# Kernel tuning notes

Hardware: AMD Instinct MI355X
Metric: run time of the kernel (lower is better)

## Reference

```python
import jax, jax.numpy as jnp
import numpy as np

LOCAL_RADIUS = 127          # block_len = 128
TOKENS_PER_BLOCK = 16       # global_seq_len = L // 16
NEG = -1e9


def _concat_3_blocks(x):
    # x: [B, nb, bl, H, d] -> [B, nb, 3*bl, H, d] (prev, cur, next block; zero-padded ends)
    p = jnp.pad(x, [(0, 0), (1, 1), (0, 0), (0, 0), (0, 0)])
    return jnp.concatenate([p[:, :-2], p[:, 1:-1], p[:, 2:]], axis=2)


def _softmax_with_extra_logit(x, axis=-1):
    m = jnp.maximum(jax.lax.stop_gradient(x.max(axis, keepdims=True)), 0)
    unnorm = jnp.exp(x - m)
    denom = unnorm.sum(axis, keepdims=True) + jnp.exp(-m)
    return unnorm / denom


def setup_inputs() -> dict:
    key = jax.random.key(0)
    ks = jax.random.split(key, 5)
    B, L, D, H, dh = 2, 4096, 1024, 16, 64
    return {
        "x": jax.random.normal(ks[0], (B, L, D), jnp.float32),
        "Wq": jax.random.normal(ks[1], (D, H, dh), jnp.float32) * 0.02,
        "Wk": jax.random.normal(ks[2], (D, H, dh), jnp.float32) * 0.02,
        "Wv": jax.random.normal(ks[3], (D, H, dh), jnp.float32) * 0.02,
        "Wo": jax.random.normal(ks[4], (H, dh, D), jnp.float32) * 0.02,
    }


def reference(x, Wq, Wk, Wv, Wo):
    B, L, D = x.shape
    H, dh = Wq.shape[1], Wq.shape[2]
    bl = LOCAL_RADIUS + 1                      # block_len = 128
    nb = L // bl                               # num_blocks
    G = L // TOKENS_PER_BLOCK                  # global (side) seq len

    q = jnp.einsum("bld,dhk->blhk", x, Wq) / jnp.sqrt(jnp.asarray(dh, x.dtype))
    k = jnp.einsum("bld,dhk->blhk", x, Wk)
    v = jnp.einsum("bld,dhk->blhk", x, Wv)

    # transient-global aggregates: sum token embeddings within each block of TOKENS_PER_BLOCK
    block_ids = jnp.arange(L) // TOKENS_PER_BLOCK          # [L]
    one_hot = jax.nn.one_hot(block_ids, G, dtype=x.dtype)  # [L, G]
    g = jnp.einsum("bld,lg->bgd", x, one_hot)              # [B, G, D]
    side_k = jnp.einsum("bgd,dhk->bghk", g, Wk)
    side_v = jnp.einsum("bgd,dhk->bghk", g, Wv)

    # split into blocks and build 3-block sliding window keys/values
    qb = q.reshape(B, nb, bl, H, dh)
    kb = _concat_3_blocks(k.reshape(B, nb, bl, H, dh))     # [B, nb, 3bl, H, dh]
    vb = _concat_3_blocks(v.reshape(B, nb, bl, H, dh))

    k_cat = jnp.concatenate(
        [kb, jnp.broadcast_to(side_k[:, None], (B, nb, G, H, dh))], axis=2)
    v_cat = jnp.concatenate(
        [vb, jnp.broadcast_to(side_v[:, None], (B, nb, G, H, dh))], axis=2)

    # logits: [B, nb, H, bl, 3bl+G]
    logits = jnp.einsum("bnqhd,bnkhd->bnhqk", qb, k_cat)

    # local mask: enforce |rel| <= local_radius and in-bounds key positions
    q_idx = jnp.arange(bl)[:, None]                        # [bl, 1]
    k_idx = jnp.arange(3 * bl)[None, :]                    # [1, 3bl]
    rel = k_idx - bl - q_idx                               # relative position
    b_idx = jnp.arange(nb)[:, None, None]                  # [nb, 1, 1]
    k_pos = (b_idx - 1) * bl + k_idx                       # absolute key position
    valid = (jnp.abs(rel) <= LOCAL_RADIUS) & (k_pos >= 0) & (k_pos < L)
    local_bias = jnp.where(valid, 0.0, NEG).astype(logits.dtype)  # [nb, bl, 3bl]
    side_bias = jnp.zeros((nb, bl, G), logits.dtype)
    bias = jnp.concatenate([local_bias, side_bias], axis=-1)      # [nb, bl, 3bl+G]
    logits = logits + bias[None, :, None]

    probs = _softmax_with_extra_logit(logits, axis=-1)
    y = jnp.einsum("bnhqk,bnkhd->bnqhd", probs, v_cat)
    y = y.reshape(B, L, H, dh)
    return jnp.einsum("blhk,hkd->bld", y, Wo)
```

## Files before the change

### kernel.cpp

```cpp
#include <hip/hip_runtime.h>
#include <stdint.h>

#define SC_LOG2E 0.18033688011112042f

typedef __attribute__((ext_vector_type(8))) short short8;
typedef __attribute__((ext_vector_type(4))) float f32x4;

__device__ __forceinline__ unsigned short f2bf(float f) {
  unsigned int u = __float_as_uint(f);
  u += 0x7fffu + ((u >> 16) & 1u);
  return (unsigned short)(u >> 16);
}

__device__ __forceinline__ void gload_lds16(const void* g, void* l) {
  __builtin_amdgcn_global_load_lds((const __attribute__((address_space(1))) void*)g,
                                   (__attribute__((address_space(3))) void*)l,
                                   16, 0, 0);
}

__device__ __forceinline__ f32x4 mfma16(short8 a, short8 b, f32x4 c) {
  return __builtin_amdgcn_mfma_f32_16x16x32_bf16(a, b, c, 0, 0, 0);
}


__global__ __launch_bounds__(256) void prep_x_k(const float* __restrict__ x,
                                                unsigned short* __restrict__ xb,
                                                unsigned short* __restrict__ gb) {
  int gr = blockIdx.x;
  int c4 = threadIdx.x;
  const float4* p = (const float4*)(x + (size_t)gr * 16384) + c4;
  float4 s = {0.f, 0.f, 0.f, 0.f};
#pragma unroll
  for (int t = 0; t < 16; ++t) {
    float4 v = p[(size_t)t * 256];
    ushort4 o;
    o.x = f2bf(v.x); o.y = f2bf(v.y); o.z = f2bf(v.z); o.w = f2bf(v.w);
    ((ushort4*)xb)[(size_t)(gr * 16 + t) * 256 + c4] = o;
    s.x += v.x; s.y += v.y; s.z += v.z; s.w += v.w;
  }
  ushort4 og;
  og.x = f2bf(s.x); og.y = f2bf(s.y); og.z = f2bf(s.z); og.w = f2bf(s.w);
  ((ushort4*)gb)[(size_t)gr * 256 + c4] = og;
}

__global__ __launch_bounds__(256) void transpose_w4_k(
    const float* __restrict__ wq, const float* __restrict__ wk,
    const float* __restrict__ wv, const float* __restrict__ wo,
    unsigned short* __restrict__ wqkv_t, unsigned short* __restrict__ wo_t) {
  __shared__ float tile[64 * 65];
  int z = blockIdx.z;
  const float* src = (z == 0) ? wq : (z == 1) ? wk : (z == 2) ? wv : wo;
  unsigned short* dst = (z == 3) ? wo_t : (wqkv_t + (size_t)z * 1048576);
  float scale = (z == 0) ? SC_LOG2E : 1.0f;
  int tc = blockIdx.x * 64, tr = blockIdx.y * 64;
  int cx = threadIdx.x & 63, ry = threadIdx.x >> 6;
#pragma unroll
  for (int i = 0; i < 16; ++i) {
    int r = ry + i * 4;
    tile[r * 65 + cx] = src[(size_t)(tr + r) * 1024 + tc + cx];
  }
  __syncthreads();
#pragma unroll
  for (int i = 0; i < 16; ++i) {
    int r = ry + i * 4;
    dst[(size_t)(tc + r) * 1024 + tr + cx] = f2bf(tile[cx * 65 + r] * scale);
  }
}

__global__ __launch_bounds__(256) void transpose_bf16_k(
    const unsigned short* __restrict__ src, int sstride, size_t szstride,
    unsigned short* __restrict__ dst, int dstride, size_t dzstride) {
  __shared__ unsigned short tile[64 * 65];
  src += blockIdx.z * szstride;
  dst += blockIdx.z * dzstride;
  int tc = blockIdx.x * 64, tr = blockIdx.y * 64;
  int cx = threadIdx.x & 63, ry = threadIdx.x >> 6;
#pragma unroll
  for (int i = 0; i < 16; ++i) {
    int r = ry + i * 4;
    tile[r * 65 + cx] = src[(size_t)(tr + r) * sstride + tc + cx];
  }
  __syncthreads();
#pragma unroll
  for (int i = 0; i < 16; ++i) {
    int r = ry + i * 4;
    dst[(size_t)(tc + r) * dstride + tr + cx] = tile[cx * 65 + r];
  }
}

template <bool F32OUT>
__global__ __launch_bounds__(256) void gemm_bt_k(
    const unsigned short* __restrict__ A, const unsigned short* __restrict__ Bt,
    void* __restrict__ Cv, int M, int N, int K, int nbn) {
  __shared__ unsigned short Alds[128 * 64];
  __shared__ unsigned short Blds[128 * 64];
  int bid = blockIdx.x;
  int bm = bid / nbn, bn = bid % nbn;
  int lane = threadIdx.x & 63, wid = threadIdx.x >> 6;
  int wr = wid >> 1, wc = wid & 1;
  int l15 = lane & 15, lg = lane >> 4;

  f32x4 zero4 = {0.f, 0.f, 0.f, 0.f};
  f32x4 acc[4][4];
#pragma unroll
  for (int i = 0; i < 4; ++i)
#pragma unroll
    for (int j = 0; j < 4; ++j) acc[i][j] = zero4;

  int srow[4], scol[4];
#pragma unroll
  for (int i = 0; i < 4; ++i) {
    int seg = wid * 4 + i;
    int r = seg * 8 + (lane >> 3);
    srow[i] = r;
    scol[i] = ((lane & 7) ^ (r & 7)) * 8;
  }
  size_t arow0 = (size_t)bm * 128, brow0 = (size_t)bn * 128;

  int ksteps = K >> 6;
  for (int ks = 0; ks < ksteps; ++ks) {
    int k0 = ks << 6;
#pragma unroll
    for (int i = 0; i < 4; ++i) {
      gload_lds16(A + (arow0 + srow[i]) * K + k0 + scol[i],
                  (char*)Alds + (wid * 4 + i) * 1024);
      gload_lds16(Bt + (brow0 + srow[i]) * K + k0 + scol[i],
                  (char*)Blds + (wid * 4 + i) * 1024);
    }
    __syncthreads();
#pragma unroll
    for (int kk = 0; kk < 2; ++kk) {
      short8 af[4], bfr[4];
#pragma unroll
      for (int mi = 0; mi < 4; ++mi) {
        int r = wr * 64 + mi * 16 + l15;
        af[mi] = *(const short8*)((const char*)Alds + r * 128 +
                                  ((kk * 64 + lg * 16) ^ ((r & 7) << 4)));
      }
#pragma unroll
      for (int ni = 0; ni < 4; ++ni) {
        int r = wc * 64 + ni * 16 + l15;
        bfr[ni] = *(const short8*)((const char*)Blds + r * 128 +
                                   ((kk * 64 + lg * 16) ^ ((r & 7) << 4)));
      }
#pragma unroll
      for (int mi = 0; mi < 4; ++mi)
#pragma unroll
        for (int ni = 0; ni < 4; ++ni)
          acc[mi][ni] = mfma16(af[mi], bfr[ni], acc[mi][ni]);
    }
    __syncthreads();
  }
  int rq = lg << 2;
#pragma unroll
  for (int mi = 0; mi < 4; ++mi) {
    size_t row = arow0 + wr * 64 + mi * 16 + rq;
#pragma unroll
    for (int ni = 0; ni < 4; ++ni) {
      size_t col = brow0 + wc * 64 + ni * 16 + l15;
#pragma unroll
      for (int r = 0; r < 4; ++r) {
        if (F32OUT)
          ((float*)Cv)[(row + r) * N + col] = acc[mi][ni][r];
        else
          ((unsigned short*)Cv)[(row + r) * N + col] = f2bf(acc[mi][ni][r]);
      }
    }
  }
}

__global__ __launch_bounds__(256) void attn_k(
    const unsigned short* __restrict__ qkv,
    const unsigned short* __restrict__ side_kv,
    const unsigned short* __restrict__ v_t,
    const unsigned short* __restrict__ side_v_t,
    unsigned short* __restrict__ y) {
  const int L = 4096, G = 256;
  __shared__ unsigned short K0[4096], V0[4096];
  __shared__ unsigned short K1[4096], V1[4096];
  __shared__ unsigned short Pl[4][2048];

  int bid = blockIdx.x;
  int n = bid & 31, h = (bid >> 5) & 15, b = bid >> 9;
  int lane = threadIdx.x & 63, wid = threadIdx.x >> 6;
  int l15 = lane & 15, lg = lane >> 4, rq = lg << 2;

  short8 qf[2][2];
  {
    size_t rowb = (size_t)b * L + n * 128 + wid * 32;
#pragma unroll
    for (int qt = 0; qt < 2; ++qt)
#pragma unroll
      for (int kk = 0; kk < 2; ++kk)
        qf[qt][kk] = *(const short8*)(qkv + (rowb + qt * 16 + l15) * 3072 +
                                      h * 64 + kk * 32 + lg * 8);
  }

  f32x4 zero4 = {0.f, 0.f, 0.f, 0.f};
  f32x4 accO[2][4], accSum[2];
#pragma unroll
  for (int qt = 0; qt < 2; ++qt) {
    accSum[qt] = zero4;
#pragma unroll
    for (int dt = 0; dt < 4; ++dt) accO[qt][dt] = zero4;
  }

  short8 onesf;
  {
    short o = (l15 == 0) ? (short)0x3F80 : (short)0;
    onesf = (short8){o, o, o, o, o, o, o, o};
  }

  int clo = (n == 0) ? 2 : 0, chi = (n == 31) ? 4 : 6;
  int nloc = chi - clo, goff = 6 - nloc;
  int m = nloc + 4;
  unsigned short* pw = Pl[wid];

  auto stage = [&](int c, unsigned short* Kl, unsigned short* Vl) {
    bool isg = c >= 6;
#pragma unroll
    for (int i = 0; i < 2; ++i) {
      int seg = wid * 2 + i;
      int r = seg * 8 + (lane >> 3);
      int sl = ((lane & 7) ^ (r & 7)) * 8;
      const unsigned short *ksrc, *vsrc;
      if (!isg) {
        int p0 = (n - 1) * 128 + c * 64;
        ksrc = qkv + (size_t)(b * L + p0 + r) * 3072 + 1024 + h * 64 + sl;
        vsrc = v_t + ((size_t)b * 1024 + h * 64 + r) * L + p0 + sl;
      } else {
        int g0 = (c - 6) * 64;
        ksrc = side_kv + (size_t)(b * G + g0 + r) * 2048 + h * 64 + sl;
        vsrc = side_v_t + ((size_t)b * 1024 + h * 64 + r) * G + g0 + sl;
      }
      gload_lds16(ksrc, (char*)Kl + seg * 1024);
      gload_lds16(vsrc, (char*)Vl + seg * 1024);
    }
  };

  auto compute = [&](int c, const unsigned short* Kl, const unsigned short* Vl) {
    bool isg = c >= 6;
    int d0 = c * 64 - 128 - wid * 32;
    if (!isg) {
      if (d0 >= 159 || d0 <= -191) return;
    }
    bool partial = !isg && !(d0 >= -96 && d0 <= 64);

    f32x4 sacc[2][4];
#pragma unroll
    for (int qt = 0; qt < 2; ++qt)
#pragma unroll
      for (int kt = 0; kt < 4; ++kt) sacc[qt][kt] = zero4;
#pragma unroll
    for (int kk = 0; kk < 2; ++kk) {
      short8 kf[4];
#pragma unroll
      for (int kt = 0; kt < 4; ++kt) {
        int r = kt * 16 + l15;
        kf[kt] = *(const short8*)((const char*)Kl + r * 128 +
                                  ((kk * 64 + lg * 16) ^ ((r & 7) << 4)));
      }
#pragma unroll
      for (int qt = 0; qt < 2; ++qt)
#pragma unroll
        for (int kt = 0; kt < 4; ++kt)
          sacc[qt][kt] = mfma16(qf[qt][kk], kf[kt], sacc[qt][kt]);
    }
    if (partial) {
      int relc = d0 + l15 - rq;
#pragma unroll
      for (int qt = 0; qt < 2; ++qt)
#pragma unroll
        for (int kt = 0; kt < 4; ++kt)
#pragma unroll
          for (int r = 0; r < 4; ++r) {
            int rel = relc + kt * 16 - qt * 16 - r;
            sacc[qt][kt][r] =
                ((unsigned)(rel + 127) <= 254u) ? sacc[qt][kt][r] : -1e30f;
          }
    }
#pragma unroll
    for (int qt = 0; qt < 2; ++qt)
#pragma unroll
      for (int kt = 0; kt < 4; ++kt)
#pragma unroll
        for (int r = 0; r < 4; ++r) {
          float p = __builtin_amdgcn_exp2f(sacc[qt][kt][r]);
          int row = qt * 16 + rq + r;
          int cb = (kt * 16 + l15) * 2;
          *(unsigned short*)((char*)pw + row * 128 +
                             (cb ^ ((row & 7) << 4))) = f2bf(p);
        }
#pragma unroll
    for (int ks = 0; ks < 2; ++ks) {
      short8 pa[2], vb[4];
#pragma unroll
      for (int qt = 0; qt < 2; ++qt) {
        int row = qt * 16 + l15;
        pa[qt] = *(const short8*)((const char*)pw + row * 128 +
                                  ((ks * 64 + lg * 16) ^ ((row & 7) << 4)));
      }
#pragma unroll
      for (int dt = 0; dt < 4; ++dt) {
        int d = dt * 16 + l15;
        vb[dt] = *(const short8*)((const char*)Vl + d * 128 +
                                  ((ks * 64 + lg * 16) ^ ((d & 7) << 4)));
      }
#pragma unroll
      for (int qt = 0; qt < 2; ++qt) {
#pragma unroll
        for (int dt = 0; dt < 4; ++dt)
          accO[qt][dt] = mfma16(pa[qt], vb[dt], accO[qt][dt]);
        accSum[qt] = mfma16(pa[qt], onesf, accSum[qt]);
      }
    }
  };

  auto chunk_of = [&](int i) { return i < nloc ? i + clo : i + goff; };

  stage(chunk_of(0), K0, V0);
  __syncthreads();
  for (int i = 0; i < m; i += 2) {
    if (i + 1 < m) stage(chunk_of(i + 1), K1, V1);
    compute(chunk_of(i), K0, V0);
    __syncthreads();
    if (i + 1 >= m) break;
    if (i + 2 < m) stage(chunk_of(i + 2), K0, V0);
    compute(chunk_of(i + 1), K1, V1);
    __syncthreads();
  }

  size_t rowb = (size_t)b * L + n * 128 + wid * 32;
#pragma unroll
  for (int qt = 0; qt < 2; ++qt) {
    float inv[4];
#pragma unroll
    for (int r = 0; r < 4; ++r) {
      float s = __shfl(accSum[qt][r], lane & 48);
      inv[r] = 1.f / (1.f + s);
    }
#pragma unroll
    for (int dt = 0; dt < 4; ++dt) {
      int col = h * 64 + dt * 16 + l15;
#pragma unroll
      for (int r = 0; r < 4; ++r)
        y[(rowb + qt * 16 + rq + r) * 1024 + col] =
            f2bf(accO[qt][dt][r] * inv[r]);
    }
  }
}

extern "C" void kernel_launch(void* const* d_in, const int* in_sizes, int n_in,
                              void* d_out, int out_size, void* d_ws, size_t ws_size,
                              hipStream_t stream) {
  const float* x  = (const float*)d_in[0];
  const float* wq = (const float*)d_in[1];
  const float* wk = (const float*)d_in[2];
  const float* wv = (const float*)d_in[3];
  const float* wo = (const float*)d_in[4];
  char* ws = (char*)d_ws;
  const size_t MB = 1 << 20;
  unsigned short* xb     = (unsigned short*)(ws);
  unsigned short* gb     = (unsigned short*)(ws + 16 * MB);
  unsigned short* wqkv_t = (unsigned short*)(ws + 17 * MB);
  unsigned short* wo_t   = (unsigned short*)(ws + 23 * MB);
  unsigned short* qkvb   = (unsigned short*)(ws + 25 * MB);
  unsigned short* sidekv = (unsigned short*)(ws + 73 * MB);
  unsigned short* vt     = (unsigned short*)(ws + 75 * MB);
  unsigned short* svt    = (unsigned short*)(ws + 91 * MB);
  unsigned short* yb     = xb;

  prep_x_k<<<512, 256, 0, stream>>>(x, xb, gb);
  transpose_w4_k<<<dim3(16, 16, 4), 256, 0, stream>>>(wq, wk, wv, wo, wqkv_t, wo_t);
  gemm_bt_k<false><<<64 * 24, 256, 0, stream>>>(xb, wqkv_t, qkvb, 8192, 3072, 1024, 24);
  gemm_bt_k<false><<<4 * 16, 256, 0, stream>>>(gb, wqkv_t + 1048576, sidekv, 512, 2048, 1024, 16);
  transpose_bf16_k<<<dim3(16, 64, 2), 256, 0, stream>>>(
      qkvb + 2048, 3072, (size_t)4096 * 3072, vt, 4096, (size_t)1024 * 4096);
  transpose_bf16_k<<<dim3(16, 4, 2), 256, 0, stream>>>(
      sidekv + 1024, 2048, (size_t)256 * 2048, svt, 256, (size_t)1024 * 256);
  attn_k<<<1024, 256, 0, stream>>>(qkvb, sidekv, vt, svt, yb);
  gemm_bt_k<true><<<64 * 8, 256, 0, stream>>>(yb, wo_t, d_out, 8192, 1024, 1024, 8);
}
```

Before: 179.1 us.

## Fuse side K/V projection into a 256x256 pipelined QKV GEMM

Adds a 512-thread GEMM kernel that uses 256x256 tiles, double-buffered LDS, staged async loads and interleaved barriers with s_setprio around MFMA phases. The side-token aggregates are appended as extra rows of the main QKV GEMM (M=8704), so one launch replaces two. The attention kernel now reads side K from the fused buffer and raises wave priority around its MFMA sections. The cost is wasted Q columns for the side rows, and workspace layout now depends on gb sitting contiguously after xb.

```diff
diff --git a/kernel.cpp b/kernel.cpp
--- a/kernel.cpp
+++ b/kernel.cpp
@@ -88,6 +88,146 @@
   }
 }
 
+__global__ __launch_bounds__(512, 2) void gemm256_k(
+    const unsigned short* __restrict__ A, const unsigned short* __restrict__ Bt,
+    unsigned short* __restrict__ C, int M, int N, int K, int nbn) {
+  __shared__ unsigned short lds[2][2][16384];
+  int nwg = gridDim.x, cpx = nwg >> 3;
+  int bid = blockIdx.x;
+  bid = (bid & 7) * cpx + (bid >> 3);
+  int bm = bid / nbn, bn = bid % nbn;
+  int lane = threadIdx.x & 63, w = threadIdx.x >> 6;
+  int wm = w >> 2, wn = w & 3;
+  int l15 = lane & 15, lg = lane >> 4;
+  int lrow = lane >> 3;
+  int lcol = ((lane & 7) ^ lrow) * 8;
+  const int KT = K >> 6;
+
+  const unsigned short* Ab = A + ((size_t)bm * 256 + lrow) * K + lcol;
+  const unsigned short* Bb = Bt + ((size_t)bn * 256 + lrow) * K + lcol;
+
+  f32x4 zero4 = {0.f, 0.f, 0.f, 0.f};
+  f32x4 acc[8][4];
+#pragma unroll
+  for (int i = 0; i < 8; ++i)
+#pragma unroll
+    for (int j = 0; j < 4; ++j) acc[i][j] = zero4;
+
+  auto stage = [&](int kind, int t) {
+    if (t >= KT) return;
+    const unsigned short* src = (kind < 2) ? Ab : Bb;
+#pragma unroll
+    for (int i = 0; i < 2; ++i) {
+      int q = i * 64 + w * 8;
+      int r0;
+      if (kind == 0)      r0 = (q & 63) + ((q >> 6) << 7);
+      else if (kind == 1) r0 = (q & 63) + ((q >> 6) << 7) + 64;
+      else if (kind == 2) r0 = (q & 31) + ((q >> 5) << 6);
+      else                r0 = (q & 31) + ((q >> 5) << 6) + 32;
+      gload_lds16(src + (size_t)r0 * K + t * 64,
+                  &lds[t & 1][kind < 2 ? 0 : 1][r0 * 64]);
+    }
+  };
+  auto ldA = [&](int p, int mi, int kk) -> short8 {
+    int r = wm * 128 + mi * 16 + l15;
+    return *(const short8*)&lds[p][0][r * 64 + ((kk * 32 + lg * 8) ^ ((r & 7) * 8))];
+  };
+  auto ldB = [&](int p, int ni, int kk) -> short8 {
+    int r = wn * 64 + ni * 16 + l15;
+    return *(const short8*)&lds[p][1][r * 64 + ((kk * 32 + lg * 8) ^ ((r & 7) * 8))];
+  };
+
+  stage(0, 0); stage(3, 0); stage(1, 0); stage(2, 0);
+  stage(0, 1); stage(3, 1); stage(1, 1);
+  asm volatile("s_waitcnt vmcnt(6)" ::: "memory");
+  __builtin_amdgcn_s_barrier();
+
+  for (int t = 0; t < KT; ++t) {
+    int p = t & 1;
+    short8 aF[4][2], b0[2][2], b1[2][2];
+#pragma unroll
+    for (int mi = 0; mi < 4; ++mi)
+#pragma unroll
+      for (int kk = 0; kk < 2; ++kk) aF[mi][kk] = ldA(p, mi, kk);
+#pragma unroll
+    for (int ni = 0; ni < 2; ++ni)
+#pragma unroll
+      for (int kk = 0; kk < 2; ++kk) b0[ni][kk] = ldB(p, ni, kk);
+    stage(2, t + 1);
+    __builtin_amdgcn_s_barrier();
+    __builtin_amdgcn_s_setprio(1);
+#pragma unroll
+    for (int mi = 0; mi < 4; ++mi)
+#pragma unroll
+      for (int ni = 0; ni < 2; ++ni)
+#pragma unroll
+        for (int kk = 0; kk < 2; ++kk)
+          acc[mi][ni] = mfma16(aF[mi][kk], b0[ni][kk], acc[mi][ni]);
+    __builtin_amdgcn_s_setprio(0);
+    __builtin_amdgcn_s_barrier();
+#pragma unroll
+    for (int ni = 0; ni < 2; ++ni)
+#pragma unroll
+      for (int kk = 0; kk < 2; ++kk) b1[ni][kk] = ldB(p, ni + 2, kk);
+    stage(0, t + 2);
+    __builtin_amdgcn_s_barrier();
+    __builtin_amdgcn_s_setprio(1);
+#pragma unroll
+    for (int mi = 0; mi < 4; ++mi)
+#pragma unroll
+      for (int ni = 0; ni < 2; ++ni)
+#pragma unroll
+        for (int kk = 0; kk < 2; ++kk)
+          acc[mi][ni + 2] = mfma16(aF[mi][kk], b1[ni][kk], acc[mi][ni + 2]);
+    __builtin_amdgcn_s_setprio(0);
+    __builtin_amdgcn_s_barrier();
+#pragma unroll
+    for (int mi = 0; mi < 4; ++mi)
+#pragma unroll
+      for (int kk = 0; kk < 2; ++kk) aF[mi][kk] = ldA(p, mi + 4, kk);
+    stage(3, t + 2);
+    __builtin_amdgcn_s_barrier();
+    __builtin_amdgcn_s_setprio(1);
+#pragma unroll
+    for (int mi = 0; mi < 4; ++mi)
+#pragma unroll
+      for (int ni = 0; ni < 2; ++ni)
+#pragma unroll
+        for (int kk = 0; kk < 2; ++kk)
+          acc[mi + 4][ni + 2] = mfma16(aF[mi][kk], b1[ni][kk], acc[mi + 4][ni + 2]);
+    __builtin_amdgcn_s_setprio(0);
+    __builtin_amdgcn_s_barrier();
+    stage(1, t + 2);
+    if (t < KT - 2)
+      asm volatile("s_waitcnt vmcnt(6)" ::: "memory");
+    else
+      asm volatile("s_waitcnt vmcnt(0)" ::: "memory");
+    __builtin_amdgcn_s_barrier();
+    __builtin_amdgcn_s_setprio(1);
+#pragma unroll
+    for (int mi = 0; mi < 4; ++mi)
+#pragma unroll
+      for (int ni = 0; ni < 2; ++ni)
+#pragma unroll
+        for (int kk = 0; kk < 2; ++kk)
+          acc[mi + 4][ni] = mfma16(aF[mi][kk], b0[ni][kk], acc[mi + 4][ni]);
+    __builtin_amdgcn_s_setprio(0);
+    __builtin_amdgcn_s_barrier();
+  }
+
+#pragma unroll
+  for (int mi = 0; mi < 8; ++mi) {
+    size_t row = (size_t)bm * 256 + wm * 128 + mi * 16 + lg * 4;
+#pragma unroll
+    for (int ni = 0; ni < 4; ++ni) {
+      size_t col = (size_t)bn * 256 + wn * 64 + ni * 16 + l15;
+#pragma unroll
+      for (int r = 0; r < 4; ++r)
+        C[(row + r) * N + col] = f2bf(acc[mi][ni][r]);
+    }
+  }
+}
+
 template <bool F32OUT>
 __global__ __launch_bounds__(256) void gemm_bt_k(
     const unsigned short* __restrict__ A, const unsigned short* __restrict__ Bt,
@@ -171,7 +311,6 @@
 
 __global__ __launch_bounds__(256) void attn_k(
     const unsigned short* __restrict__ qkv,
-    const unsigned short* __restrict__ side_kv,
     const unsigned short* __restrict__ v_t,
     const unsigned short* __restrict__ side_v_t,
     unsigned short* __restrict__ y) {
@@ -230,7 +369,7 @@
         vsrc = v_t + ((size_t)b * 1024 + h * 64 + r) * L + p0 + sl;
       } else {
         int g0 = (c - 6) * 64;
-        ksrc = side_kv + (size_t)(b * G + g0 + r) * 2048 + h * 64 + sl;
+        ksrc = qkv + (size_t)(8192 + b * G + g0 + r) * 3072 + 1024 + h * 64 + sl;
         vsrc = side_v_t + ((size_t)b * 1024 + h * 64 + r) * G + g0 + sl;
       }
       gload_lds16(ksrc, (char*)Kl + seg * 1024);
@@ -251,6 +390,7 @@
     for (int qt = 0; qt < 2; ++qt)
 #pragma unroll
       for (int kt = 0; kt < 4; ++kt) sacc[qt][kt] = zero4;
+    __builtin_amdgcn_s_setprio(1);
 #pragma unroll
     for (int kk = 0; kk < 2; ++kk) {
       short8 kf[4];
@@ -266,6 +406,7 @@
         for (int kt = 0; kt < 4; ++kt)
           sacc[qt][kt] = mfma16(qf[qt][kk], kf[kt], sacc[qt][kt]);
     }
+    __builtin_amdgcn_s_setprio(0);
     if (partial) {
       int relc = d0 + l15 - rq;
 #pragma unroll
@@ -291,6 +432,7 @@
           *(unsigned short*)((char*)pw + row * 128 +
                              (cb ^ ((row & 7) << 4))) = f2bf(p);
         }
+    __builtin_amdgcn_s_setprio(1);
 #pragma unroll
     for (int ks = 0; ks < 2; ++ks) {
       short8 pa[2], vb[4];
@@ -314,6 +456,7 @@
         accSum[qt] = mfma16(pa[qt], onesf, accSum[qt]);
       }
     }
+    __builtin_amdgcn_s_setprio(0);
   };
 
   auto chunk_of = [&](int i) { return i < nloc ? i + clo : i + goff; };
@@ -365,19 +508,18 @@
   unsigned short* wqkv_t = (unsigned short*)(ws + 17 * MB);
   unsigned short* wo_t   = (unsigned short*)(ws + 23 * MB);
   unsigned short* qkvb   = (unsigned short*)(ws + 25 * MB);
-  unsigned short* sidekv = (unsigned short*)(ws + 73 * MB);
-  unsigned short* vt     = (unsigned short*)(ws + 75 * MB);
-  unsigned short* svt    = (unsigned short*)(ws + 91 * MB);
+  unsigned short* vt     = (unsigned short*)(ws + 76 * MB);
+  unsigned short* svt    = gb;
   unsigned short* yb     = xb;
 
   prep_x_k<<<512, 256, 0, stream>>>(x, xb, gb);
   transpose_w4_k<<<dim3(16, 16, 4), 256, 0, stream>>>(wq, wk, wv, wo, wqkv_t, wo_t);
-  gemm_bt_k<false><<<64 * 24, 256, 0, stream>>>(xb, wqkv_t, qkvb, 8192, 3072, 1024, 24);
-  gemm_bt_k<false><<<4 * 16, 256, 0, stream>>>(gb, wqkv_t + 1048576, sidekv, 512, 2048, 1024, 16);
+  gemm256_k<<<34 * 12, 512, 0, stream>>>(xb, wqkv_t, qkvb, 8704, 3072, 1024, 12);
   transpose_bf16_k<<<dim3(16, 64, 2), 256, 0, stream>>>(
       qkvb + 2048, 3072, (size_t)4096 * 3072, vt, 4096, (size_t)1024 * 4096);
   transpose_bf16_k<<<dim3(16, 4, 2), 256, 0, stream>>>(
-      sidekv + 1024, 2048, (size_t)256 * 2048, svt, 256, (size_t)1024 * 256);
-  attn_k<<<1024, 256, 0, stream>>>(qkvb, sidekv, vt, svt, yb);
+      qkvb + (size_t)8192 * 3072 + 2048, 3072, (size_t)256 * 3072, svt, 256,
+      (size_t)1024 * 256);
+  attn_k<<<1024, 256, 0, stream>>>(qkvb, vt, svt, yb);
   gemm_bt_k<true><<<64 * 8, 256, 0, stream>>>(yb, wo_t, d_out, 8192, 1024, 1024, 8);
 }
```

Measured after the change: 162.1 us. 9.5% less time.

## Drop V transpose kernels via LDS transpose reads and fuse side-KV GEMM

Applied to the files above, without the earlier changes.

Removes the two bf16 transpose kernels for V and side-V. V is now staged into LDS in row-major order in a permuted layout and read back with ds_read_b64_tr_b16 to form the PV MFMA operands. The side K/V projection is folded into the main QKV GEMM by extending M to cover the global-token rows, which sit contiguously after x in the workspace. This also computes some unused side-Q columns. MFMA sections are wrapped in s_setprio raises, and an explicit lgkmcnt wait is added before the PV MFMAs.

```diff
diff --git a/kernel.cpp b/kernel.cpp
--- a/kernel.cpp
+++ b/kernel.cpp
@@ -4,6 +4,7 @@
 #define SC_LOG2E 0.18033688011112042f
 
 typedef __attribute__((ext_vector_type(8))) short short8;
+typedef __attribute__((ext_vector_type(4))) short short4v;
 typedef __attribute__((ext_vector_type(4))) float f32x4;
 
 __device__ __forceinline__ unsigned short f2bf(float f) {
@@ -20,6 +21,18 @@
 
 __device__ __forceinline__ f32x4 mfma16(short8 a, short8 b, f32x4 c) {
   return __builtin_amdgcn_mfma_f32_16x16x32_bf16(a, b, c, 0, 0, 0);
+}
+
+__device__ __forceinline__ short4v tr_read(const unsigned short* p) {
+  short4v r;
+  asm volatile("ds_read_b64_tr_b16 %0, %1"
+               : "=v"(r)
+               : "v"((const __attribute__((address_space(3))) unsigned short*)p));
+  return r;
+}
+
+__device__ __forceinline__ short8 cat44(short4v lo, short4v hi) {
+  return __builtin_shufflevector(lo, hi, 0, 1, 2, 3, 4, 5, 6, 7);
 }
 
 
@@ -67,27 +80,6 @@
   }
 }
 
-__global__ __launch_bounds__(256) void transpose_bf16_k(
-    const unsigned short* __restrict__ src, int sstride, size_t szstride,
-    unsigned short* __restrict__ dst, int dstride, size_t dzstride) {
-  __shared__ unsigned short tile[64 * 65];
-  src += blockIdx.z * szstride;
-  dst += blockIdx.z * dzstride;
-  int tc = blockIdx.x * 64, tr = blockIdx.y * 64;
-  int cx = threadIdx.x & 63, ry = threadIdx.x >> 6;
-#pragma unroll
-  for (int i = 0; i < 16; ++i) {
-    int r = ry + i * 4;
-    tile[r * 65 + cx] = src[(size_t)(tr + r) * sstride + tc + cx];
-  }
-  __syncthreads();
-#pragma unroll
-  for (int i = 0; i < 16; ++i) {
-    int r = ry + i * 4;
-    dst[(size_t)(tc + r) * dstride + tr + cx] = tile[cx * 65 + r];
-  }
-}
-
 template <bool F32OUT>
 __global__ __launch_bounds__(256) void gemm_bt_k(
     const unsigned short* __restrict__ A, const unsigned short* __restrict__ Bt,
@@ -171,9 +163,6 @@
 
 __global__ __launch_bounds__(256) void attn_k(
     const unsigned short* __restrict__ qkv,
-    const unsigned short* __restrict__ side_kv,
-    const unsigned short* __restrict__ v_t,
-    const unsigned short* __restrict__ side_v_t,
     unsigned short* __restrict__ y) {
   const int L = 4096, G = 256;
   __shared__ unsigned short K0[4096], V0[4096];
@@ -218,23 +207,24 @@
 
   auto stage = [&](int c, unsigned short* Kl, unsigned short* Vl) {
     bool isg = c >= 6;
+    int rowbase;
+    if (!isg)
+      rowbase = b * L + (n - 1) * 128 + c * 64;
+    else
+      rowbase = 8192 + b * G + (c - 6) * 64;
 #pragma unroll
     for (int i = 0; i < 2; ++i) {
       int seg = wid * 2 + i;
       int r = seg * 8 + (lane >> 3);
       int sl = ((lane & 7) ^ (r & 7)) * 8;
-      const unsigned short *ksrc, *vsrc;
-      if (!isg) {
-        int p0 = (n - 1) * 128 + c * 64;
-        ksrc = qkv + (size_t)(b * L + p0 + r) * 3072 + 1024 + h * 64 + sl;
-        vsrc = v_t + ((size_t)b * 1024 + h * 64 + r) * L + p0 + sl;
-      } else {
-        int g0 = (c - 6) * 64;
-        ksrc = side_kv + (size_t)(b * G + g0 + r) * 2048 + h * 64 + sl;
-        vsrc = side_v_t + ((size_t)b * 1024 + h * 64 + r) * G + g0 + sl;
-      }
-      gload_lds16(ksrc, (char*)Kl + seg * 1024);
-      gload_lds16(vsrc, (char*)Vl + seg * 1024);
+      gload_lds16(qkv + (size_t)(rowbase + r) * 3072 + 1024 + h * 64 + sl,
+                  (char*)Kl + seg * 1024);
+      int S = seg * 8 + (lane >> 3);
+      int di = S >> 4, ks = (S >> 3) & 1, lgg = (S >> 1) & 3, half = S & 1;
+      int k = ks * 32 + lgg * 8 + half * 4 + ((lane & 7) >> 1);
+      int d = di * 16 + (lane & 1) * 8;
+      gload_lds16(qkv + (size_t)(rowbase + k) * 3072 + 2048 + h * 64 + d,
+                  (char*)Vl + seg * 1024);
     }
   };
 
@@ -251,6 +241,7 @@
     for (int qt = 0; qt < 2; ++qt)
 #pragma unroll
       for (int kt = 0; kt < 4; ++kt) sacc[qt][kt] = zero4;
+    __builtin_amdgcn_s_setprio(1);
 #pragma unroll
     for (int kk = 0; kk < 2; ++kk) {
       short8 kf[4];
@@ -266,6 +257,7 @@
         for (int kt = 0; kt < 4; ++kt)
           sacc[qt][kt] = mfma16(qf[qt][kk], kf[kt], sacc[qt][kt]);
     }
+    __builtin_amdgcn_s_setprio(0);
     if (partial) {
       int relc = d0 + l15 - rq;
 #pragma unroll
@@ -293,26 +285,32 @@
         }
 #pragma unroll
     for (int ks = 0; ks < 2; ++ks) {
-      short8 pa[2], vb[4];
+      short8 pa[2];
 #pragma unroll
       for (int qt = 0; qt < 2; ++qt) {
         int row = qt * 16 + l15;
         pa[qt] = *(const short8*)((const char*)pw + row * 128 +
                                   ((ks * 64 + lg * 16) ^ ((row & 7) << 4)));
       }
+      short4v vlo[4], vhi[4];
 #pragma unroll
       for (int dt = 0; dt < 4; ++dt) {
-        int d = dt * 16 + l15;
-        vb[dt] = *(const short8*)((const char*)Vl + d * 128 +
-                                  ((ks * 64 + lg * 16) ^ ((d & 7) << 4)));
-      }
+        const unsigned short* base =
+            Vl + (((dt * 2 + ks) * 4 + lg) * 2) * 64 + l15 * 4;
+        vlo[dt] = tr_read(base);
+        vhi[dt] = tr_read(base + 64);
+      }
+      asm volatile("s_waitcnt lgkmcnt(0)" ::: "memory");
+      __builtin_amdgcn_sched_barrier(0);
+      __builtin_amdgcn_s_setprio(1);
 #pragma unroll
       for (int qt = 0; qt < 2; ++qt) {
 #pragma unroll
         for (int dt = 0; dt < 4; ++dt)
-          accO[qt][dt] = mfma16(pa[qt], vb[dt], accO[qt][dt]);
+          accO[qt][dt] = mfma16(pa[qt], cat44(vlo[dt], vhi[dt]), accO[qt][dt]);
         accSum[qt] = mfma16(pa[qt], onesf, accSum[qt]);
       }
+      __builtin_amdgcn_s_setprio(0);
     }
   };
 
@@ -365,19 +363,11 @@
   unsigned short* wqkv_t = (unsigned short*)(ws + 17 * MB);
   unsigned short* wo_t   = (unsigned short*)(ws + 23 * MB);
   unsigned short* qkvb   = (unsigned short*)(ws + 25 * MB);
-  unsigned short* sidekv = (unsigned short*)(ws + 73 * MB);
-  unsigned short* vt     = (unsigned short*)(ws + 75 * MB);
-  unsigned short* svt    = (unsigned short*)(ws + 91 * MB);
   unsigned short* yb     = xb;
 
   prep_x_k<<<512, 256, 0, stream>>>(x, xb, gb);
   transpose_w4_k<<<dim3(16, 16, 4), 256, 0, stream>>>(wq, wk, wv, wo, wqkv_t, wo_t);
-  gemm_bt_k<false><<<64 * 24, 256, 0, stream>>>(xb, wqkv_t, qkvb, 8192, 3072, 1024, 24);
-  gemm_bt_k<false><<<4 * 16, 256, 0, stream>>>(gb, wqkv_t + 1048576, sidekv, 512, 2048, 1024, 16);
-  transpose_bf16_k<<<dim3(16, 64, 2), 256, 0, stream>>>(
-      qkvb + 2048, 3072, (size_t)4096 * 3072, vt, 4096, (size_t)1024 * 4096);
-  transpose_bf16_k<<<dim3(16, 4, 2), 256, 0, stream>>>(
-      sidekv + 1024, 2048, (size_t)256 * 2048, svt, 256, (size_t)1024 * 256);
-  attn_k<<<1024, 256, 0, stream>>>(qkvb, sidekv, vt, svt, yb);
+  gemm_bt_k<false><<<68 * 24, 256, 0, stream>>>(xb, wqkv_t, qkvb, 8704, 3072, 1024, 24);
+  attn_k<<<1024, 256, 0, stream>>>(qkvb, yb);
   gemm_bt_k<true><<<64 * 8, 256, 0, stream>>>(yb, wo_t, d_out, 8192, 1024, 1024, 8);
 }
```

Result: faster. 161.9 us (-9.6%).
